# Kernel optimization log

Measured on AMD Instinct MI355X. Metric: run time of the kernel, lower is better.

## Reference

```python
import jax, jax.numpy as jnp
import numpy as np

B, S, D, H = 2, 2048, 768, 12
DK = D // H


def setup_inputs() -> dict:
    key = jax.random.key(0)
    ks = jax.random.split(key, 13)
    s = 0.02
    return {
        "query": jax.random.normal(ks[0], (B, S, D), jnp.float32),
        "key": jax.random.normal(ks[1], (B, S, D), jnp.float32),
        "mask": jax.random.randint(ks[2], (B, S, S), 0, 2, jnp.int32),
        "short": jax.random.normal(ks[3], (B, H, S, S), jnp.float32),
        "aspect": jax.random.normal(ks[4], (B, D), jnp.float32),
        "Wq": jax.random.normal(ks[5], (D, D), jnp.float32) * s,
        "bq": jax.random.normal(ks[6], (D,), jnp.float32) * s,
        "Wk": jax.random.normal(ks[7], (D, D), jnp.float32) * s,
        "bk": jax.random.normal(ks[8], (D,), jnp.float32) * s,
        "Wd": jax.random.normal(ks[9], (D, DK), jnp.float32) * s,
        "bd": jax.random.normal(ks[10], (DK,), jnp.float32) * s,
        "weight_m": jax.random.normal(ks[11], (H, DK, DK), jnp.float32) * s,
        "bias_m": jax.random.normal(ks[12], (1,), jnp.float32) * s,
    }


def reference(query, key, mask, short, aspect, Wq, bq, Wk, bk, Wd, bd, weight_m, bias_m):
    b, sq, d = query.shape
    h, dk = weight_m.shape[0], weight_m.shape[1]
    # projections -> [B, H, S, DK]
    q = (query @ Wq + bq).reshape(b, sq, h, dk).transpose(0, 2, 1, 3)
    k = (key @ Wk + bk).reshape(b, -1, h, dk).transpose(0, 2, 1, 3)
    scores = jnp.einsum("bhsd,bhtd->bhst", q, k) / jnp.sqrt(jnp.float32(dk))
    # aspect path: same per-head vector broadcast over query positions
    a = aspect @ Wd + bd                                  # [B, DK]
    am = jnp.einsum("bd,hde->bhe", a, weight_m)           # [B, H, DK]
    aspect_scores = jnp.tanh(
        jnp.einsum("bhe,bhte->bht", am, k)[:, :, None, :] + bias_m
    )                                                      # [B, H, 1, S] broadcasts over s
    scores = scores + aspect_scores
    m = mask[:, :, :sq][:, None, :, :]                     # [B, 1, S, S]
    scores = jnp.where(m == 0, jnp.float32(-1e9), scores)
    scores = scores + short
    return jax.nn.softmax(scores, axis=-1)
```

## Files before the change

### kernel.cpp

```cpp
#include <hip/hip_runtime.h>
#include <math.h>

#define BB 2
#define SS 2048
#define DD 768
#define HH 12
#define DKK 64
#define BH (BB*HH)

typedef __attribute__((ext_vector_type(8))) __bf16 bf16x8;
typedef __attribute__((ext_vector_type(4))) float floatx4;
typedef __attribute__((ext_vector_type(4))) int intx4;
typedef unsigned short ushort_t;
typedef __attribute__((ext_vector_type(4))) unsigned short ushortx4;

__device__ inline float bf2f(ushort_t u) {
    unsigned int x = ((unsigned int)u) << 16;
    return __builtin_bit_cast(float, x);
}
__device__ inline ushort_t f2bf(float f) {
    unsigned int x = __builtin_bit_cast(unsigned int, f);
    unsigned int lsb = (x >> 16) & 1u;
    x += 0x7fffu + lsb;
    return (ushort_t)(x >> 16);
}

template<int ISBF>
__device__ inline float ldf(const void* p, size_t i) {
    if (ISBF) return bf2f(((const ushort_t*)p)[i]);
    else      return ((const float*)p)[i];
}

__global__ void detect_dtype(const ushort_t* __restrict__ q, int* __restrict__ flag) {
    __shared__ int cnt;
    if (threadIdx.x == 0) cnt = 0;
    __syncthreads();
    ushort_t u = q[2 * threadIdx.x];
    int e = (u >> 7) & 0xFF;
    if (e >= 0x66 && e <= 0x84) atomicAdd(&cnt, 1);
    __syncthreads();
    if (threadIdx.x == 0) *flag = (cnt >= 128) ? 1 : 0;
}

template<int ISBF>
__device__ void transpose_body(const void* __restrict__ in, ushort_t* __restrict__ out) {
    int t = blockIdx.x * 256 + threadIdx.x;
    if (t >= DD * DD) return;
    int e = t / DD, d = t - e * DD;
    out[t] = f2bf(ldf<ISBF>(in, (size_t)d * DD + e));
}
__global__ void transpose_w(const void* in, ushort_t* out, const int* flag) {
    if (*flag) transpose_body<1>(in, out); else transpose_body<0>(in, out);
}

template<int ISBF>
__device__ void gemm_body(const void* __restrict__ A, const ushort_t* __restrict__ Wt,
                          const void* __restrict__ bias, ushort_t* __restrict__ outp,
                          ushort_t* lAs, ushort_t* lBs)
{
    const int tid = threadIdx.x;
    const int lane = tid & 63, wave = tid >> 6;
    const int quad = lane >> 4, l15 = lane & 15;
    const int wm = wave >> 1, wn = wave & 1;
    const int r0 = blockIdx.y * 128;
    const int n0 = blockIdx.x * 128;

    floatx4 acc[4][4];
    #pragma unroll
    for (int m = 0; m < 4; m++)
        #pragma unroll
        for (int n = 0; n < 4; n++) acc[m][n] = (floatx4){0.f, 0.f, 0.f, 0.f};

    for (int kb = 0; kb < DD / 64; ++kb) {
        const int k0 = kb * 64;
        __syncthreads();
        #pragma unroll
        for (int i = 0; i < 4; i++) {
            int idx = tid + i * 256;
            int r = idx >> 3, c = idx & 7;
            int gc = c ^ (r & 7);
            size_t aoff = (size_t)(r0 + r) * DD + k0 + gc * 8;
            bf16x8 va;
            if (ISBF) {
                va = *(const bf16x8*)((const ushort_t*)A + aoff);
            } else {
                const float* Af = (const float*)A;
                floatx4 f0 = *(const floatx4*)(Af + aoff);
                floatx4 f1 = *(const floatx4*)(Af + aoff + 4);
                union { ushort_t u[8]; bf16x8 v; } t;
                #pragma unroll
                for (int j = 0; j < 4; j++) { t.u[j] = f2bf(f0[j]); t.u[4 + j] = f2bf(f1[j]); }
                va = t.v;
            }
            *(bf16x8*)(lAs + r * 64 + c * 8) = va;
            bf16x8 vb = *(const bf16x8*)(Wt + (size_t)(n0 + r) * DD + k0 + gc * 8);
            *(bf16x8*)(lBs + r * 64 + c * 8) = vb;
        }
        __syncthreads();
        #pragma unroll
        for (int kc = 0; kc < 2; kc++) {
            bf16x8 af[4], bfr[4];
            #pragma unroll
            for (int m = 0; m < 4; m++) {
                int row = wm * 64 + m * 16 + l15;
                int chunk = (kc * 4 + quad) ^ (row & 7);
                af[m] = *(const bf16x8*)(lAs + row * 64 + chunk * 8);
            }
            #pragma unroll
            for (int n = 0; n < 4; n++) {
                int row = wn * 64 + n * 16 + l15;
                int chunk = (kc * 4 + quad) ^ (row & 7);
                bfr[n] = *(const bf16x8*)(lBs + row * 64 + chunk * 8);
            }
            #pragma unroll
            for (int m = 0; m < 4; m++)
                #pragma unroll
                for (int n = 0; n < 4; n++)
                    acc[m][n] = __builtin_amdgcn_mfma_f32_16x16x32_bf16(af[m], bfr[n], acc[m][n], 0, 0, 0);
        }
    }
    #pragma unroll
    for (int n = 0; n < 4; n++) {
        int E = n0 + wn * 64 + n * 16 + l15;
        float bv = ldf<ISBF>(bias, E);
        int h = E >> 6, dk = E & 63;
        #pragma unroll
        for (int m = 0; m < 4; m++) {
            #pragma unroll
            for (int j = 0; j < 4; j++) {
                int R = r0 + wm * 64 + m * 16 + quad * 4 + j;
                int b = R >> 11, s = R & 2047;
                float v = acc[m][n][j] + bv;
                outp[(((size_t)(b * HH + h)) * SS + s) * DKK + dk] = f2bf(v);
            }
        }
    }
}
__global__ __launch_bounds__(256, 2) void gemm_proj(
    const void* A, const ushort_t* Wt, const void* bias, ushort_t* outp, const int* flag)
{
    __shared__ __align__(16) ushort_t lAs[128 * 64];
    __shared__ __align__(16) ushort_t lBs[128 * 64];
    if (*flag) gemm_body<1>(A, Wt, bias, outp, lAs, lBs);
    else       gemm_body<0>(A, Wt, bias, outp, lAs, lBs);
}

template<int ISBF>
__device__ void aspect_body(const void* __restrict__ aspect, const void* __restrict__ Wd,
                            const void* __restrict__ bd, const void* __restrict__ wm,
                            float* __restrict__ am_out, float* a_sh)
{
    int tid = threadIdx.x;
    if (tid < BB * DKK) {
        int b = tid >> 6, dk = tid & 63;
        float s = 0.f;
        for (int d = 0; d < DD; ++d)
            s += ldf<ISBF>(aspect, b * DD + d) * ldf<ISBF>(Wd, (size_t)d * DKK + dk);
        s += ldf<ISBF>(bd, dk);
        a_sh[tid] = s;
    }
    __syncthreads();
    for (int idx = tid; idx < BB * HH * DKK; idx += 256) {
        int b = idx / (HH * DKK);
        int rem = idx - b * (HH * DKK);
        int h = rem >> 6, e = rem & 63;
        float s = 0.f;
        for (int dk = 0; dk < DKK; ++dk)
            s += a_sh[b * DKK + dk] * ldf<ISBF>(wm, (size_t)(h * DKK + dk) * DKK + e);
        am_out[idx] = s;
    }
}
__global__ void aspect_am(const void* aspect, const void* Wd, const void* bd,
                          const void* wm, float* am_out, const int* flag) {
    __shared__ float a_sh[BB * DKK];
    if (*flag) aspect_body<1>(aspect, Wd, bd, wm, am_out, a_sh);
    else       aspect_body<0>(aspect, Wd, bd, wm, am_out, a_sh);
}

template<int ISBF>
__device__ void ascore_body(const float* __restrict__ am, const ushort_t* __restrict__ kws,
                            const void* __restrict__ bias_m, float* __restrict__ asc) {
    int idx = blockIdx.x * 256 + threadIdx.x;
    if (idx >= BH * SS) return;
    int bh = idx >> 11;
    int t = idx & 2047;
    const float* amv = am + bh * DKK;
    const ushort_t* kp = kws + ((size_t)bh * SS + t) * DKK;
    float s = 0.f;
    #pragma unroll
    for (int e0 = 0; e0 < DKK; e0 += 8) {
        union { bf16x8 v; ushort_t u[8]; } t8;
        t8.v = *(const bf16x8*)(kp + e0);
        #pragma unroll
        for (int j = 0; j < 8; j++) s += amv[e0 + j] * bf2f(t8.u[j]);
    }
    s += ldf<ISBF>(bias_m, 0);
    asc[idx] = tanhf(s);
}
__global__ void ascore_k(const float* am, const ushort_t* kws, const void* bias_m,
                         float* asc, const int* flag) {
    if (*flag) ascore_body<1>(am, kws, bias_m, asc);
    else       ascore_body<0>(am, kws, bias_m, asc);
}

template<int ISBF>
__device__ void scores_body(const ushort_t* __restrict__ qws, const ushort_t* __restrict__ kws,
                            const float* __restrict__ asc, const int* __restrict__ mask,
                            const void* __restrict__ shr, void* __restrict__ outv,
                            float (*red)[16])
{
    const int tid = threadIdx.x;
    const int lane = tid & 63, wave = tid >> 6;
    const int quad = lane >> 4, l15 = lane & 15;
    const int r0 = blockIdx.x * 16;
    const int bh = blockIdx.y;
    const int b = bh / HH;

    const ushort_t* qp = qws + ((size_t)bh * SS + r0) * DKK;
    const ushort_t* kp = kws + ((size_t)bh * SS) * DKK;

    bf16x8 bq0 = *(const bf16x8*)(qp + l15 * DKK + quad * 8);
    bf16x8 bq1 = *(const bf16x8*)(qp + l15 * DKK + 32 + quad * 8);

    const int c0 = wave * 128;
    floatx4 acc[8];
    #pragma unroll
    for (int i = 0; i < 8; i++) {
        const ushort_t* kt = kp + (size_t)(c0 + i * 16 + l15) * DKK + quad * 8;
        bf16x8 a0 = *(const bf16x8*)(kt);
        bf16x8 a1 = *(const bf16x8*)(kt + 32);
        floatx4 a = (floatx4){0.f, 0.f, 0.f, 0.f};
        a = __builtin_amdgcn_mfma_f32_16x16x32_bf16(a0, bq0, a, 0, 0, 0);
        a = __builtin_amdgcn_mfma_f32_16x16x32_bf16(a1, bq1, a, 0, 0, 0);
        acc[i] = a;
    }

    const int r = r0 + l15;
    const float* ascp  = asc + (size_t)bh * SS;
    const int*   maskp = mask + ((size_t)(b * SS + r)) * SS;
    const size_t rowoff = ((size_t)(bh * SS + r)) * SS;

    float mx = -3.0e38f;
    #pragma unroll
    for (int i = 0; i < 8; i++) {
        int ct = c0 + i * 16 + quad * 4;
        floatx4 av = *(const floatx4*)(ascp + ct);
        intx4   mk = *(const intx4*)(maskp + ct);
        floatx4 sv;
        if (ISBF) {
            ushortx4 s4 = *(const ushortx4*)((const ushort_t*)shr + rowoff + ct);
            #pragma unroll
            for (int j = 0; j < 4; j++) sv[j] = bf2f(s4[j]);
        } else {
            sv = *(const floatx4*)((const float*)shr + rowoff + ct);
        }
        #pragma unroll
        for (int j = 0; j < 4; j++) {
            float s = (mk[j] == 0) ? -1e9f : (acc[i][j] * 0.125f + av[j]);
            s += sv[j];
            acc[i][j] = s;
            mx = fmaxf(mx, s);
        }
    }
    mx = fmaxf(mx, __shfl_xor(mx, 16));
    mx = fmaxf(mx, __shfl_xor(mx, 32));
    if (lane < 16) red[wave][lane] = mx;
    __syncthreads();
    float rmax = red[0][l15];
    #pragma unroll
    for (int w = 1; w < 16; w++) rmax = fmaxf(rmax, red[w][l15]);
    __syncthreads();

    float sm = 0.f;
    #pragma unroll
    for (int i = 0; i < 8; i++)
        #pragma unroll
        for (int j = 0; j < 4; j++) {
            float p = __expf(acc[i][j] - rmax);
            acc[i][j] = p;
            sm += p;
        }
    sm += __shfl_xor(sm, 16);
    sm += __shfl_xor(sm, 32);
    if (lane < 16) red[wave][lane] = sm;
    __syncthreads();
    float tot = red[0][l15];
    #pragma unroll
    for (int w = 1; w < 16; w++) tot += red[w][l15];
    float rinv = 1.0f / tot;

    #pragma unroll
    for (int i = 0; i < 8; i++) {
        int ct = c0 + i * 16 + quad * 4;
        size_t oidx = rowoff + ct;
        if (ISBF) {
            ushortx4 o4;
            #pragma unroll
            for (int j = 0; j < 4; j++) o4[j] = f2bf(acc[i][j] * rinv);
            *(ushortx4*)((ushort_t*)outv + oidx) = o4;
        } else {
            floatx4 o4;
            #pragma unroll
            for (int j = 0; j < 4; j++) o4[j] = acc[i][j] * rinv;
            *(floatx4*)((float*)outv + oidx) = o4;
        }
    }
}
__global__ __launch_bounds__(1024, 4) void scores_softmax(
    const ushort_t* qws, const ushort_t* kws, const float* asc, const int* mask,
    const void* shr, void* outv, const int* flag)
{
    __shared__ float red[16][16];
    if (*flag) scores_body<1>(qws, kws, asc, mask, shr, outv, red);
    else       scores_body<0>(qws, kws, asc, mask, shr, outv, red);
}

extern "C" void kernel_launch(void* const* d_in, const int* in_sizes, int n_in,
                              void* d_out, int out_size, void* d_ws, size_t ws_size,
                              hipStream_t stream) {
    const void* query  = d_in[0];
    const void* key    = d_in[1];
    const int*  mask   = (const int*)d_in[2];
    const void* shr    = d_in[3];
    const void* aspect = d_in[4];
    const void* Wq     = d_in[5];
    const void* bq     = d_in[6];
    const void* Wk     = d_in[7];
    const void* bk     = d_in[8];
    const void* Wd     = d_in[9];
    const void* bd     = d_in[10];
    const void* wm     = d_in[11];
    const void* bias_m = d_in[12];

    char* ws = (char*)d_ws;
    const size_t QK_BYTES = (size_t)BH * SS * DKK * 2;
    const size_t WT_BYTES = (size_t)DD * DD * 2;
    ushort_t* qws = (ushort_t*)(ws);
    ushort_t* kws = (ushort_t*)(ws + QK_BYTES);
    ushort_t* wtq = (ushort_t*)(ws + 2 * QK_BYTES);
    ushort_t* wtk = (ushort_t*)(ws + 2 * QK_BYTES + WT_BYTES);
    float*    amb = (float*)   (ws + 2 * QK_BYTES + 2 * WT_BYTES);
    float*    asc = (float*)   (ws + 2 * QK_BYTES + 2 * WT_BYTES + 8192);
    int*      flg = (int*)     (ws + 2 * QK_BYTES + 2 * WT_BYTES + 8192 + (size_t)BH * SS * 4);

    detect_dtype<<<1, 256, 0, stream>>>((const ushort_t*)query, flg);
    transpose_w<<<dim3((DD * DD + 255) / 256), 256, 0, stream>>>(Wq, wtq, flg);
    transpose_w<<<dim3((DD * DD + 255) / 256), 256, 0, stream>>>(Wk, wtk, flg);
    gemm_proj<<<dim3(DD / 128, (BB * SS) / 128), 256, 0, stream>>>(query, wtq, bq, qws, flg);
    gemm_proj<<<dim3(DD / 128, (BB * SS) / 128), 256, 0, stream>>>(key,   wtk, bk, kws, flg);
    aspect_am<<<1, 256, 0, stream>>>(aspect, Wd, bd, wm, amb, flg);
    ascore_k<<<dim3((BH * SS + 255) / 256), 256, 0, stream>>>(amb, kws, bias_m, asc, flg);
    scores_softmax<<<dim3(SS / 16, BH), 1024, 0, stream>>>(qws, kws, asc, mask, shr, d_out, flg);
}
```

Measured before the change: 959.5 us.

## Transpose score tiles through LDS for coalesced softmax and merge Q/K projection GEMMs

The scores kernel now stages MFMA accumulators through a swizzled LDS buffer so each wave owns one full row. Mask, short and output accesses become lane-contiguous and coalesced, and the row reduction stays inside the wave with shuffles instead of cross-wave LDS reductions. The Q and K projection GEMMs are merged into one launch using blockIdx.z, with the tile shrunk from 128 to 64 to give more blocks. The trade-offs are extra LDS round trips and barriers in the scores kernel, scalar rather than vector global loads, and lower launch-bounds occupancy.

```diff
diff --git a/kernel.cpp b/kernel.cpp
--- a/kernel.cpp
+++ b/kernel.cpp
@@ -10,9 +10,7 @@
 
 typedef __attribute__((ext_vector_type(8))) __bf16 bf16x8;
 typedef __attribute__((ext_vector_type(4))) float floatx4;
-typedef __attribute__((ext_vector_type(4))) int intx4;
 typedef unsigned short ushort_t;
-typedef __attribute__((ext_vector_type(4))) unsigned short ushortx4;
 
 __device__ inline float bf2f(ushort_t u) {
     unsigned int x = ((unsigned int)u) << 16;
@@ -62,24 +60,24 @@
     const int lane = tid & 63, wave = tid >> 6;
     const int quad = lane >> 4, l15 = lane & 15;
     const int wm = wave >> 1, wn = wave & 1;
-    const int r0 = blockIdx.y * 128;
-    const int n0 = blockIdx.x * 128;
-
-    floatx4 acc[4][4];
-    #pragma unroll
-    for (int m = 0; m < 4; m++)
-        #pragma unroll
-        for (int n = 0; n < 4; n++) acc[m][n] = (floatx4){0.f, 0.f, 0.f, 0.f};
+    const int r0 = blockIdx.y * 64;
+    const int n0 = blockIdx.x * 64;
+
+    floatx4 acc[2][2];
+    #pragma unroll
+    for (int m = 0; m < 2; m++)
+        #pragma unroll
+        for (int n = 0; n < 2; n++) acc[m][n] = (floatx4){0.f, 0.f, 0.f, 0.f};
 
     for (int kb = 0; kb < DD / 64; ++kb) {
         const int k0 = kb * 64;
         __syncthreads();
         #pragma unroll
-        for (int i = 0; i < 4; i++) {
+        for (int i = 0; i < 2; i++) {
             int idx = tid + i * 256;
-            int r = idx >> 3, c = idx & 7;
-            int gc = c ^ (r & 7);
-            size_t aoff = (size_t)(r0 + r) * DD + k0 + gc * 8;
+            int rr = idx >> 3, c = idx & 7;
+            int gc = c ^ (rr & 7);
+            size_t aoff = (size_t)(r0 + rr) * DD + k0 + gc * 8;
             bf16x8 va;
             if (ISBF) {
                 va = *(const bf16x8*)((const ushort_t*)A + aoff);
@@ -92,43 +90,43 @@
                 for (int j = 0; j < 4; j++) { t.u[j] = f2bf(f0[j]); t.u[4 + j] = f2bf(f1[j]); }
                 va = t.v;
             }
-            *(bf16x8*)(lAs + r * 64 + c * 8) = va;
-            bf16x8 vb = *(const bf16x8*)(Wt + (size_t)(n0 + r) * DD + k0 + gc * 8);
-            *(bf16x8*)(lBs + r * 64 + c * 8) = vb;
+            *(bf16x8*)(lAs + rr * 64 + c * 8) = va;
+            bf16x8 vb = *(const bf16x8*)(Wt + (size_t)(n0 + rr) * DD + k0 + gc * 8);
+            *(bf16x8*)(lBs + rr * 64 + c * 8) = vb;
         }
         __syncthreads();
         #pragma unroll
         for (int kc = 0; kc < 2; kc++) {
-            bf16x8 af[4], bfr[4];
+            bf16x8 af[2], bfr[2];
             #pragma unroll
-            for (int m = 0; m < 4; m++) {
-                int row = wm * 64 + m * 16 + l15;
+            for (int m = 0; m < 2; m++) {
+                int row = wm * 32 + m * 16 + l15;
                 int chunk = (kc * 4 + quad) ^ (row & 7);
                 af[m] = *(const bf16x8*)(lAs + row * 64 + chunk * 8);
             }
             #pragma unroll
-            for (int n = 0; n < 4; n++) {
-                int row = wn * 64 + n * 16 + l15;
+            for (int n = 0; n < 2; n++) {
+                int row = wn * 32 + n * 16 + l15;
                 int chunk = (kc * 4 + quad) ^ (row & 7);
                 bfr[n] = *(const bf16x8*)(lBs + row * 64 + chunk * 8);
             }
             #pragma unroll
-            for (int m = 0; m < 4; m++)
+            for (int m = 0; m < 2; m++)
                 #pragma unroll
-                for (int n = 0; n < 4; n++)
+                for (int n = 0; n < 2; n++)
                     acc[m][n] = __builtin_amdgcn_mfma_f32_16x16x32_bf16(af[m], bfr[n], acc[m][n], 0, 0, 0);
         }
     }
     #pragma unroll
-    for (int n = 0; n < 4; n++) {
-        int E = n0 + wn * 64 + n * 16 + l15;
+    for (int n = 0; n < 2; n++) {
+        int E = n0 + wn * 32 + n * 16 + l15;
         float bv = ldf<ISBF>(bias, E);
         int h = E >> 6, dk = E & 63;
         #pragma unroll
-        for (int m = 0; m < 4; m++) {
+        for (int m = 0; m < 2; m++) {
             #pragma unroll
             for (int j = 0; j < 4; j++) {
-                int R = r0 + wm * 64 + m * 16 + quad * 4 + j;
+                int R = r0 + wm * 32 + m * 16 + quad * 4 + j;
                 int b = R >> 11, s = R & 2047;
                 float v = acc[m][n][j] + bv;
                 outp[(((size_t)(b * HH + h)) * SS + s) * DKK + dk] = f2bf(v);
@@ -136,11 +134,16 @@
         }
     }
 }
-__global__ __launch_bounds__(256, 2) void gemm_proj(
-    const void* A, const ushort_t* Wt, const void* bias, ushort_t* outp, const int* flag)
-{
-    __shared__ __align__(16) ushort_t lAs[128 * 64];
-    __shared__ __align__(16) ushort_t lBs[128 * 64];
+__global__ __launch_bounds__(256, 4) void gemm_proj(
+    const void* q, const void* k, const ushort_t* wtq, const ushort_t* wtk,
+    const void* bq, const void* bk, ushort_t* qws, ushort_t* kws, const int* flag)
+{
+    __shared__ __align__(16) ushort_t lAs[64 * 64];
+    __shared__ __align__(16) ushort_t lBs[64 * 64];
+    const void* A      = blockIdx.z ? k   : q;
+    const ushort_t* Wt = blockIdx.z ? wtk : wtq;
+    const void* bias   = blockIdx.z ? bk  : bq;
+    ushort_t* outp     = blockIdx.z ? kws : qws;
     if (*flag) gemm_body<1>(A, Wt, bias, outp, lAs, lBs);
     else       gemm_body<0>(A, Wt, bias, outp, lAs, lBs);
 }
@@ -207,7 +210,7 @@
 __device__ void scores_body(const ushort_t* __restrict__ qws, const ushort_t* __restrict__ kws,
                             const float* __restrict__ asc, const int* __restrict__ mask,
                             const void* __restrict__ shr, void* __restrict__ outv,
-                            float (*red)[16])
+                            float* lds)
 {
     const int tid = threadIdx.x;
     const int lane = tid & 63, wave = tid >> 6;
@@ -222,11 +225,11 @@
     bf16x8 bq0 = *(const bf16x8*)(qp + l15 * DKK + quad * 8);
     bf16x8 bq1 = *(const bf16x8*)(qp + l15 * DKK + 32 + quad * 8);
 
-    const int c0 = wave * 128;
     floatx4 acc[8];
     #pragma unroll
     for (int i = 0; i < 8; i++) {
-        const ushort_t* kt = kp + (size_t)(c0 + i * 16 + l15) * DKK + quad * 8;
+        int ct0 = wave * 16 + i * 256;
+        const ushort_t* kt = kp + (size_t)(ct0 + l15) * DKK + quad * 8;
         bf16x8 a0 = *(const bf16x8*)(kt);
         bf16x8 a1 = *(const bf16x8*)(kt + 32);
         floatx4 a = (floatx4){0.f, 0.f, 0.f, 0.f};
@@ -235,84 +238,72 @@
         acc[i] = a;
     }
 
-    const int r = r0 + l15;
+    const int r = r0 + wave;
     const float* ascp  = asc + (size_t)bh * SS;
     const int*   maskp = mask + ((size_t)(b * SS + r)) * SS;
     const size_t rowoff = ((size_t)(bh * SS + r)) * SS;
 
+    const int l7 = l15 & 7;
+    const int w7 = wave & 7;
+    const int ln4 = lane >> 2, lm4 = lane & 3;
+
+    float* wr0 = lds + l15 * 512 + (((4 * wave + quad) ^ l7) << 2);
+    float* wr1 = wr0 + 256;
+    const int rbase = wave * 512 + ((lane & 32) ? 32 : 0)
+                    + (((ln4 & 7) ^ w7) << 2) + lm4;
+
+    float v[32];
     float mx = -3.0e38f;
     #pragma unroll
-    for (int i = 0; i < 8; i++) {
-        int ct = c0 + i * 16 + quad * 4;
-        floatx4 av = *(const floatx4*)(ascp + ct);
-        intx4   mk = *(const intx4*)(maskp + ct);
-        floatx4 sv;
-        if (ISBF) {
-            ushortx4 s4 = *(const ushortx4*)((const ushort_t*)shr + rowoff + ct);
-            #pragma unroll
-            for (int j = 0; j < 4; j++) sv[j] = bf2f(s4[j]);
-        } else {
-            sv = *(const floatx4*)((const float*)shr + rowoff + ct);
-        }
-        #pragma unroll
-        for (int j = 0; j < 4; j++) {
-            float s = (mk[j] == 0) ? -1e9f : (acc[i][j] * 0.125f + av[j]);
-            s += sv[j];
-            acc[i][j] = s;
+    for (int ci = 0; ci < 4; ci++) {
+        __syncthreads();
+        *(floatx4*)wr0 = acc[2 * ci + 0];
+        *(floatx4*)wr1 = acc[2 * ci + 1];
+        __syncthreads();
+        const int cb = ci * 512;
+        #pragma unroll
+        for (int kk = 0; kk < 8; kk++) {
+            int c = cb + kk * 64 + lane;
+            float sraw = lds[rbase + kk * 64];
+            float av = ascp[c];
+            int mk = maskp[c];
+            float sv = ldf<ISBF>(shr, rowoff + c);
+            float s = (mk == 0) ? -1e9f : (sraw * 0.125f + av);
+            s += sv;
+            v[ci * 8 + kk] = s;
             mx = fmaxf(mx, s);
         }
     }
-    mx = fmaxf(mx, __shfl_xor(mx, 16));
-    mx = fmaxf(mx, __shfl_xor(mx, 32));
-    if (lane < 16) red[wave][lane] = mx;
-    __syncthreads();
-    float rmax = red[0][l15];
-    #pragma unroll
-    for (int w = 1; w < 16; w++) rmax = fmaxf(rmax, red[w][l15]);
-    __syncthreads();
-
+    #pragma unroll
+    for (int off = 1; off < 64; off <<= 1) mx = fmaxf(mx, __shfl_xor(mx, off));
     float sm = 0.f;
     #pragma unroll
-    for (int i = 0; i < 8; i++)
-        #pragma unroll
-        for (int j = 0; j < 4; j++) {
-            float p = __expf(acc[i][j] - rmax);
-            acc[i][j] = p;
-            sm += p;
-        }
-    sm += __shfl_xor(sm, 16);
-    sm += __shfl_xor(sm, 32);
-    if (lane < 16) red[wave][lane] = sm;
-    __syncthreads();
-    float tot = red[0][l15];
-    #pragma unroll
-    for (int w = 1; w < 16; w++) tot += red[w][l15];
-    float rinv = 1.0f / tot;
-
-    #pragma unroll
-    for (int i = 0; i < 8; i++) {
-        int ct = c0 + i * 16 + quad * 4;
-        size_t oidx = rowoff + ct;
-        if (ISBF) {
-            ushortx4 o4;
-            #pragma unroll
-            for (int j = 0; j < 4; j++) o4[j] = f2bf(acc[i][j] * rinv);
-            *(ushortx4*)((ushort_t*)outv + oidx) = o4;
-        } else {
-            floatx4 o4;
-            #pragma unroll
-            for (int j = 0; j < 4; j++) o4[j] = acc[i][j] * rinv;
-            *(floatx4*)((float*)outv + oidx) = o4;
-        }
-    }
-}
-__global__ __launch_bounds__(1024, 4) void scores_softmax(
+    for (int t = 0; t < 32; t++) {
+        float p = __expf(v[t] - mx);
+        v[t] = p;
+        sm += p;
+    }
+    #pragma unroll
+    for (int off = 1; off < 64; off <<= 1) sm += __shfl_xor(sm, off);
+    float rinv = 1.0f / sm;
+
+    #pragma unroll
+    for (int ci = 0; ci < 4; ci++)
+        #pragma unroll
+        for (int kk = 0; kk < 8; kk++) {
+            int c = ci * 512 + kk * 64 + lane;
+            float o = v[ci * 8 + kk] * rinv;
+            if (ISBF) ((ushort_t*)outv)[rowoff + c] = f2bf(o);
+            else      ((float*)outv)[rowoff + c] = o;
+        }
+}
+__global__ __launch_bounds__(1024, 1) void scores_softmax(
     const ushort_t* qws, const ushort_t* kws, const float* asc, const int* mask,
     const void* shr, void* outv, const int* flag)
 {
-    __shared__ float red[16][16];
-    if (*flag) scores_body<1>(qws, kws, asc, mask, shr, outv, red);
-    else       scores_body<0>(qws, kws, asc, mask, shr, outv, red);
+    __shared__ __align__(16) float lds[16 * 512];
+    if (*flag) scores_body<1>(qws, kws, asc, mask, shr, outv, lds);
+    else       scores_body<0>(qws, kws, asc, mask, shr, outv, lds);
 }
 
 extern "C" void kernel_launch(void* const* d_in, const int* in_sizes, int n_in,
@@ -346,8 +337,8 @@
     detect_dtype<<<1, 256, 0, stream>>>((const ushort_t*)query, flg);
     transpose_w<<<dim3((DD * DD + 255) / 256), 256, 0, stream>>>(Wq, wtq, flg);
     transpose_w<<<dim3((DD * DD + 255) / 256), 256, 0, stream>>>(Wk, wtk, flg);
-    gemm_proj<<<dim3(DD / 128, (BB * SS) / 128), 256, 0, stream>>>(query, wtq, bq, qws, flg);
-    gemm_proj<<<dim3(DD / 128, (BB * SS) / 128), 256, 0, stream>>>(key,   wtk, bk, kws, flg);
+    gemm_proj<<<dim3(DD / 64, (BB * SS) / 64, 2), 256, 0, stream>>>(
+        query, key, wtq, wtk, bq, bk, qws, kws, flg);
     aspect_am<<<1, 256, 0, stream>>>(aspect, Wd, bd, wm, amb, flg);
     ascore_k<<<dim3((BH * SS + 255) / 256), 256, 0, stream>>>(amb, kws, bias_m, asc, flg);
     scores_softmax<<<dim3(SS / 16, BH), 1024, 0, stream>>>(qws, kws, asc, mask, shr, d_out, flg);
```

New measurement: 1.001 ms. 4.3% more time.
